# Performance work log

Hardware: AMD Instinct MI355X
Metric: run time of the kernel (lower is better)

Reference implementation:

```python
import jax, jax.numpy as jnp
import numpy as np

HIDDEN = 1024
BATCH = 16
SEQ = 2048
NEG_INF = -1000000000.0


def setup_inputs() -> dict:
    key = jax.random.key(0)
    k1, k2, k3, k4, k5, k6, k7 = jax.random.split(key, 7)
    scale = 1.0 / np.sqrt(HIDDEN)
    return {
        "query": jax.random.normal(k1, (BATCH, HIDDEN), dtype=jnp.float32),
        "keys": jax.random.normal(k2, (BATCH, SEQ, HIDDEN), dtype=jnp.float32),
        "values": jax.random.normal(k3, (BATCH, SEQ, HIDDEN), dtype=jnp.float32),
        "mask": jax.random.randint(k4, (BATCH, SEQ), 0, 2, dtype=jnp.int32),
        # Learned params (nn.Linear(in, out) weight has shape (out, in); we store transposed for x @ W)
        "W1": jax.random.uniform(k5, (HIDDEN, HIDDEN), dtype=jnp.float32, minval=-scale, maxval=scale),
        "W2": jax.random.uniform(k6, (HIDDEN, HIDDEN), dtype=jnp.float32, minval=-scale, maxval=scale),
        "v": jax.random.uniform(k7, (HIDDEN,), dtype=jnp.float32, minval=-scale, maxval=scale),
    }


def reference(query, keys, values, mask, W1, W2, v):
    # scores = v^T tanh(W1 q + W2 k)
    q_proj = query @ W1                       # (b, h)
    k_proj = jnp.einsum('bsh,hd->bsd', keys, W2)  # (b, s, h)
    scores = jnp.einsum('bsh,h->bs', jnp.tanh(q_proj[:, None, :] + k_proj), v)  # (b, s)
    scores = jnp.where(mask == 0, NEG_INF, scores)
    attention_weights = jax.nn.softmax(scores, axis=1)  # (b, s)
    context = jnp.einsum('bs,bsh->bh', attention_weights, values)  # (b, h)
    return context, attention_weights
```

## Files before the change

kernel.cpp:

```cpp
#include <hip/hip_runtime.h>
#include <hip/hip_bf16.h>
#include <cstdint>
#include <cstddef>

#define HIDDEN 1024
#define BATCH 16
#define SEQ 2048
#define M_TOTAL (BATCH*SEQ)
#define NEG_INF -1000000000.0f

typedef unsigned short u16;
typedef __bf16 bf16x8 __attribute__((ext_vector_type(8)));
typedef unsigned short u16x8 __attribute__((ext_vector_type(8)));
typedef unsigned short u16x4 __attribute__((ext_vector_type(4)));
typedef float f32x4 __attribute__((ext_vector_type(4)));

typedef const __attribute__((address_space(1))) void* gas_ptr;
typedef __attribute__((address_space(3))) void* las_ptr;

__device__ __forceinline__ u16 f2bf(float f) {
    unsigned int x = __float_as_uint(f);
    unsigned int r = (x + 0x7fffu + ((x >> 16) & 1u)) >> 16;
    return (u16)r;
}

__device__ __forceinline__ unsigned cvt_pk_bf16(float lo, float hi) {
    unsigned r;
    asm("v_cvt_pk_bf16_f32 %0, %1, %2" : "=v"(r) : "v"(lo), "v"(hi));
    return r;
}

__device__ __forceinline__ float fast_tanh(float x) {
    float e = __expf(2.0f * x);
    return 1.0f - 2.0f / (e + 1.0f);
}

__global__ __launch_bounds__(512) void qproj_kernel(
    const float* __restrict__ q, const float* __restrict__ W1,
    float* __restrict__ qp)
{
    const int b  = blockIdx.y;
    const int tl = threadIdx.x & 63;
    const int kc = threadIdx.x >> 6;
    const int n  = blockIdx.x * 64 + tl;
    __shared__ float red[8][64];

    const float* qrow = q + b * HIDDEN;
    float acc = 0.f;
    #pragma unroll 8
    for (int k = kc * 128; k < kc * 128 + 128; ++k)
        acc += qrow[k] * W1[(size_t)k * HIDDEN + n];
    red[kc][tl] = acc;
    __syncthreads();
    if (kc == 0) {
        float s = 0.f;
        #pragma unroll
        for (int i = 0; i < 8; ++i) s += red[i][tl];
        qp[b * HIDDEN + n] = s;
    }
}

__global__ __launch_bounds__(256) void w2t_kernel(
    const float* __restrict__ W2, u16* __restrict__ W2T)
{
    __shared__ float tile[64][65];
    const int n0 = blockIdx.x * 64, k0 = blockIdx.y * 64;
    const int tid = threadIdx.x;
    const int c = tid & 63, rb = tid >> 6;
    #pragma unroll
    for (int i = 0; i < 16; ++i) {
        int r = rb + i * 4;
        tile[r][c] = W2[(size_t)(k0 + r) * HIDDEN + n0 + c];
    }
    __syncthreads();
    #pragma unroll
    for (int i = 0; i < 16; ++i) {
        int r = rb + i * 4;
        W2T[(size_t)(n0 + r) * HIDDEN + k0 + c] = f2bf(tile[c][r]);
    }
}

#define NT4 16

#define WAITV(N) asm volatile("s_waitcnt vmcnt(" #N ")" ::: "memory")
#define WAITLGKM0 asm volatile("s_waitcnt lgkmcnt(0)" ::: "memory")

#define SBAR() do { __builtin_amdgcn_s_barrier(); \
                    asm volatile("" ::: "memory"); } while (0)

#define A_LOAD(DST, HALF, KT)                                               \
    do {                                                                    \
        _Pragma("unroll")                                                   \
        for (int h_ = 0; h_ < 4; ++h_)                                      \
            DST[h_] = *(const float4*)(keys                                 \
                + (size_t)(m0 + (HALF) * 128 + arow + h_ * 32) * HIDDEN     \
                + (KT) + ac * 4);                                           \
    } while (0)

#define A_WRITE(SRC, LOFF)                                                  \
    do {                                                                    \
        _Pragma("unroll")                                                   \
        for (int h_ = 0; h_ < 4; ++h_) {                                    \
            int row_ = arow + h_ * 32;                                      \
            unsigned lo_ = cvt_pk_bf16(SRC[h_].x, SRC[h_].y);               \
            unsigned hi_ = cvt_pk_bf16(SRC[h_].z, SRC[h_].w);               \
            int byte_ = row_ * 128 + (((ac >> 1) ^ (row_ & 7)) << 4)        \
                        + ((ac & 1) << 3);                                  \
            *(uint2*)((char*)lds + (LOFF) + byte_) = make_uint2(lo_, hi_);  \
        }                                                                   \
    } while (0)

#define STAGE_B(ROW0, KT, LOFF)                                             \
    do {                                                                    \
        _Pragma("unroll")                                                   \
        for (int r_ = 0; r_ < 2; ++r_) {                                    \
            int idx_ = r_ * 512 + tid;                                      \
            int row_ = idx_ >> 3, c_ = idx_ & 7;                            \
            const u16* s_ = W2T + (size_t)(n0 + (ROW0) + row_) * HIDDEN     \
                            + (KT) + ((c_ ^ (row_ & 7)) << 3);              \
            las_ptr d_ = (las_ptr)((char*)lds + (LOFF)                      \
                            + (size_t)(r_ * 512 + (wave << 6)) * 16);       \
            __builtin_amdgcn_global_load_lds((gas_ptr)s_, d_, 16, 0, 0);    \
        }                                                                   \
    } while (0)

#define LDFRAG(LBASE, ROWL, CH) __builtin_bit_cast(bf16x8,                  \
    *(const u16x8*)((LBASE) + (ROWL) * 64 + ((((CH) ^ ((ROWL) & 7))) << 3)))

#define PHASE(MS, NS, LOADA, ...)                                           \
    do {                                                                    \
        if (LOADA) {                                                        \
            _Pragma("unroll")                                               \
            for (int i_ = 0; i_ < 4; ++i_) {                                \
                int rowa_ = (MS) * 128 + wr * 64 + i_ * 16 + c16;           \
                af[i_][0] = LDFRAG(Acur, rowa_, quad);                      \
                af[i_][1] = LDFRAG(Acur, rowa_, 4 + quad);                  \
            }                                                               \
        }                                                                   \
        _Pragma("unroll")                                                   \
        for (int jj_ = 0; jj_ < 2; ++jj_) {                                 \
            int rowb_ = (NS) * 128 + wc * 32 + jj_ * 16 + c16;              \
            bfr[jj_][0] = LDFRAG(Bcur, rowb_, quad);                        \
            bfr[jj_][1] = LDFRAG(Bcur, rowb_, 4 + quad);                    \
        }                                                                   \
        __VA_ARGS__;                                                        \
        SBAR();                                                             \
        __builtin_amdgcn_s_setprio(1);                                      \
        _Pragma("unroll")                                                   \
        for (int i_ = 0; i_ < 4; ++i_)                                      \
            _Pragma("unroll")                                               \
            for (int jj_ = 0; jj_ < 2; ++jj_) {                             \
                acc[MS][i_][NS][jj_] =                                      \
                    __builtin_amdgcn_mfma_f32_16x16x32_bf16(                \
                        af[i_][0], bfr[jj_][0], acc[MS][i_][NS][jj_],0,0,0);\
                acc[MS][i_][NS][jj_] =                                      \
                    __builtin_amdgcn_mfma_f32_16x16x32_bf16(                \
                        af[i_][1], bfr[jj_][1], acc[MS][i_][NS][jj_],0,0,0);\
            }                                                               \
        __builtin_amdgcn_s_setprio(0);                                      \
        SBAR();                                                             \
    } while (0)

__global__ __launch_bounds__(512) void scores_v4_kernel(
    const float* __restrict__ keys,
    const u16*   __restrict__ W2T,
    const float* __restrict__ qp,
    const float* __restrict__ v,
    float*       __restrict__ part)
{
    __shared__ __align__(16) u16 lds[65536];

    const int tid = threadIdx.x;
    const int lid = blockIdx.x + (blockIdx.y << 2);
    const int xcd = lid & 7;
    const int j8  = lid >> 3;
    const int nt  = j8 & 3;
    const int mt  = (xcd << 4) + (j8 >> 2);
    const int m0  = mt << 8;
    const int n0  = nt << 8;

    const int wave = tid >> 6, lane = tid & 63;
    const int wr = wave >> 2;
    const int wc = wave & 3;
    const int quad = lane >> 4, c16 = lane & 15;

    const int arow = tid >> 4;
    const int ac   = tid & 15;

    f32x4 acc[2][4][2][2];
    #pragma unroll
    for (int a = 0; a < 2; ++a)
        #pragma unroll
        for (int i = 0; i < 4; ++i)
            #pragma unroll
            for (int c = 0; c < 2; ++c)
                #pragma unroll
                for (int d = 0; d < 2; ++d)
                    acc[a][i][c][d] = f32x4{0.f, 0.f, 0.f, 0.f};

    bf16x8 af[4][2], bfr[2][2];
    float4 a0[4], a1[4];

    A_LOAD(a0, 0, 0);
    STAGE_B(0, 0, 65536);
    A_LOAD(a1, 1, 0);
    STAGE_B(128, 0, 65536 + 16384);
    WAITV(8);
    A_WRITE(a0, 0);
    WAITV(2);
    A_WRITE(a1, 16384);
    WAITV(0);
    WAITLGKM0;
    SBAR();

    for (int T = 0; T < NT4 - 1; ++T) {
        const int p = T & 1;
        const u16* Acur = (const u16*)((const char*)lds + p * 32768);
        const u16* Bcur = (const u16*)((const char*)lds + 65536 + p * 32768);
        const int aoff = (p ^ 1) * 32768;
        const int boff = 65536 + (p ^ 1) * 32768;
        const int ktn = (T + 1) * 64;

        PHASE(0, 0, true,
              A_LOAD(a0, 0, ktn); STAGE_B(0, ktn, boff); WAITV(6));
        PHASE(0, 1, false,
              WAITV(2); A_WRITE(a0, aoff);
              A_LOAD(a1, 1, ktn); STAGE_B(128, ktn, boff + 16384));
        PHASE(1, 0, true,
              WAITV(2); A_WRITE(a1, aoff + 16384));
        PHASE(1, 1, false,
              WAITLGKM0);
    }
    {
        const u16* Acur = (const u16*)((const char*)lds + 32768);
        const u16* Bcur = (const u16*)((const char*)lds + 65536 + 32768);
        PHASE(0, 0, true,  WAITV(0));
        PHASE(0, 1, false, );
        PHASE(1, 0, true,  );
        PHASE(1, 1, false, );
    }

    const int b = m0 >> 11;
    float qv[2][2], vv[2][2];
    #pragma unroll
    for (int ns = 0; ns < 2; ++ns)
        #pragma unroll
        for (int jj = 0; jj < 2; ++jj) {
            int n = n0 + ns * 128 + wc * 32 + jj * 16 + c16;
            qv[ns][jj] = qp[b * HIDDEN + n];
            vv[ns][jj] = v[n];
        }
    const int slot = (nt << 2) + wc;
    #pragma unroll
    for (int ms = 0; ms < 2; ++ms)
        #pragma unroll
        for (int i = 0; i < 4; ++i)
            #pragma unroll
            for (int r = 0; r < 4; ++r) {
                float s = 0.f;
                #pragma unroll
                for (int ns = 0; ns < 2; ++ns)
                    #pragma unroll
                    for (int jj = 0; jj < 2; ++jj)
                        s += fast_tanh(acc[ms][i][ns][jj][r] + qv[ns][jj])
                             * vv[ns][jj];
                s += __shfl_xor(s, 1);
                s += __shfl_xor(s, 2);
                s += __shfl_xor(s, 4);
                s += __shfl_xor(s, 8);
                if (c16 == 0) {
                    int m = m0 + ms * 128 + wr * 64 + i * 16 + quad * 4 + r;
                    part[(size_t)slot * M_TOTAL + m] = s;
                }
            }
}

#define BM 128
#define BN 128
#define BK 64
#define LDA 72

__global__ __launch_bounds__(256) void scores_v1_kernel(
    const float* __restrict__ keys,
    const u16*   __restrict__ W2T,
    const float* __restrict__ qp,
    const float* __restrict__ v,
    float*       __restrict__ part)
{
    __shared__ __align__(16) u16 Alds[BM][LDA];
    __shared__ __align__(16) u16 Blds[BN][LDA];

    const int tid  = threadIdx.x;
    const int nt   = blockIdx.x;
    const int n0   = nt * BN;
    const int m0   = blockIdx.y * BM;
    const int wave = tid >> 6, lane = tid & 63;
    const int wr = wave >> 1, wc = wave & 1;
    const int quad = lane >> 4, c16 = lane & 15;

    f32x4 acc[4][4];
    #pragma unroll
    for (int i = 0; i < 4; ++i)
        #pragma unroll
        for (int jj = 0; jj < 4; ++jj)
            acc[i][jj] = f32x4{0.f, 0.f, 0.f, 0.f};

    for (int kt = 0; kt < HIDDEN; kt += BK) {
        __syncthreads();
        const float* gA = keys + (size_t)m0 * HIDDEN + kt;
        #pragma unroll
        for (int i = 0; i < 8; ++i) {
            int idx = tid + i * 256;
            int r = idx >> 4, c4 = idx & 15;
            float4 f = *(const float4*)(gA + (size_t)r * HIDDEN + c4 * 4);
            u16x4 pk;
            pk[0] = f2bf(f.x); pk[1] = f2bf(f.y);
            pk[2] = f2bf(f.z); pk[3] = f2bf(f.w);
            *(u16x4*)&Alds[r][c4 * 4] = pk;
        }
        #pragma unroll
        for (int i = 0; i < 4; ++i) {
            int idx = tid + i * 256;
            int r = idx >> 3, c8 = idx & 7;
            uint4 raw = ((const uint4*)(W2T + (size_t)(n0 + r) * HIDDEN + kt))[c8];
            *(uint4*)&Blds[r][c8 * 8] = raw;
        }
        __syncthreads();

        #pragma unroll
        for (int ks = 0; ks < BK; ks += 32) {
            bf16x8 af[4], bfr[4];
            #pragma unroll
            for (int i = 0; i < 4; ++i)
                af[i] = __builtin_bit_cast(bf16x8,
                    *(const u16x8*)&Alds[wr * 64 + i * 16 + c16][ks + quad * 8]);
            #pragma unroll
            for (int jj = 0; jj < 4; ++jj)
                bfr[jj] = __builtin_bit_cast(bf16x8,
                    *(const u16x8*)&Blds[wc * 64 + jj * 16 + c16][ks + quad * 8]);
            #pragma unroll
            for (int i = 0; i < 4; ++i)
                #pragma unroll
                for (int jj = 0; jj < 4; ++jj)
                    acc[i][jj] = __builtin_amdgcn_mfma_f32_16x16x32_bf16(
                        af[i], bfr[jj], acc[i][jj], 0, 0, 0);
        }
    }

    const int b = m0 >> 11;
    float qv[4], vv[4];
    #pragma unroll
    for (int jj = 0; jj < 4; ++jj) {
        int n = n0 + wc * 64 + jj * 16 + c16;
        qv[jj] = qp[b * HIDDEN + n];
        vv[jj] = v[n];
    }
    const int slot = nt * 2 + wc;
    #pragma unroll
    for (int i = 0; i < 4; ++i) {
        #pragma unroll
        for (int r = 0; r < 4; ++r) {
            float s = 0.f;
            #pragma unroll
            for (int jj = 0; jj < 4; ++jj)
                s += fast_tanh(acc[i][jj][r] + qv[jj]) * vv[jj];
            s += __shfl_xor(s, 1);
            s += __shfl_xor(s, 2);
            s += __shfl_xor(s, 4);
            s += __shfl_xor(s, 8);
            if (c16 == 0) {
                int m = m0 + wr * 64 + i * 16 + quad * 4 + r;
                part[(size_t)slot * M_TOTAL + m] = s;
            }
        }
    }
}

__global__ __launch_bounds__(1024) void softmax_kernel(
    const float* __restrict__ part, const int* __restrict__ mask,
    float* __restrict__ attn)
{
    const int b = blockIdx.x, tid = threadIdx.x;
    const int wave = tid >> 6, lane = tid & 63;
    __shared__ float red[16];
    float sc[2];
    float mx = -1e30f;
    #pragma unroll
    for (int j = 0; j < 2; ++j) {
        int s = tid + j * 1024;
        float a = 0.f;
        #pragma unroll
        for (int p = 0; p < 16; ++p)
            a += part[(size_t)p * M_TOTAL + b * SEQ + s];
        if (mask[b * SEQ + s] == 0) a = NEG_INF;
        sc[j] = a;
        mx = fmaxf(mx, a);
    }
    #pragma unroll
    for (int o = 32; o > 0; o >>= 1) mx = fmaxf(mx, __shfl_xor(mx, o));
    if (lane == 0) red[wave] = mx;
    __syncthreads();
    #pragma unroll
    for (int w = 0; w < 16; ++w) mx = fmaxf(mx, red[w]);
    float sum = 0.f;
    #pragma unroll
    for (int j = 0; j < 2; ++j) { sc[j] = __expf(sc[j] - mx); sum += sc[j]; }
    #pragma unroll
    for (int o = 32; o > 0; o >>= 1) sum += __shfl_xor(sum, o);
    __syncthreads();
    if (lane == 0) red[wave] = sum;
    __syncthreads();
    sum = 0.f;
    #pragma unroll
    for (int w = 0; w < 16; ++w) sum += red[w];
    float inv = 1.0f / sum;
    #pragma unroll
    for (int j = 0; j < 2; ++j)
        attn[b * SEQ + tid + j * 1024] = sc[j] * inv;
}

__global__ __launch_bounds__(256) void ctx_part_kernel(
    const float* __restrict__ values, const float* __restrict__ attn,
    float* __restrict__ ctxp)
{
    const int b = blockIdx.x, sch = blockIdx.y, tid = threadIdx.x;
    __shared__ float w[32];
    if (tid < 32) w[tid] = attn[b * SEQ + sch * 32 + tid];
    __syncthreads();
    float4 acc = {0.f, 0.f, 0.f, 0.f};
    const float4* V = (const float4*)(values
        + (size_t)b * SEQ * HIDDEN + (size_t)sch * 32 * HIDDEN);
    #pragma unroll 4
    for (int s = 0; s < 32; ++s) {
        float wv = w[s];
        if (wv != 0.0f) {
            float4 x = V[(size_t)s * (HIDDEN / 4) + tid];
            acc.x += wv * x.x; acc.y += wv * x.y;
            acc.z += wv * x.z; acc.w += wv * x.w;
        }
    }
    ((float4*)(ctxp + (size_t)(b * 64 + sch) * HIDDEN))[tid] = acc;
}

__global__ __launch_bounds__(256) void ctx_reduce_kernel(
    const float* __restrict__ ctxp, float* __restrict__ ctx)
{
    const int b = blockIdx.x, tid = threadIdx.x;
    float4 acc = {0.f, 0.f, 0.f, 0.f};
    const float4* P = (const float4*)(ctxp + (size_t)b * 64 * HIDDEN);
    #pragma unroll 8
    for (int s = 0; s < 64; ++s) {
        float4 x = P[(size_t)s * (HIDDEN / 4) + tid];
        acc.x += x.x; acc.y += x.y; acc.z += x.z; acc.w += x.w;
    }
    ((float4*)(ctx + (size_t)b * HIDDEN))[tid] = acc;
}

extern "C" void kernel_launch(void* const* d_in, const int* in_sizes, int n_in,
                              void* d_out, int out_size, void* d_ws, size_t ws_size,
                              hipStream_t stream)
{
    const float* query  = (const float*)d_in[0];
    const float* keys   = (const float*)d_in[1];
    const float* values = (const float*)d_in[2];
    const int*   mask   = (const int*)d_in[3];
    const float* W1     = (const float*)d_in[4];
    const float* W2     = (const float*)d_in[5];
    const float* v      = (const float*)d_in[6];
    float* out = (float*)d_out;

    char* ws = (char*)d_ws;
    float* qp     = (float*)ws;
    u16*   w2t    = (u16*)(ws + (64 << 10));
    float* part   = (float*)(ws + (64 << 10) + (2 << 20));
    float* ctxp   = (float*)(ws + (64 << 10) + (4 << 20));
    const size_t WS_V4 = (64 << 10) + (8 << 20);

    float* attn_out = out + BATCH * HIDDEN;

    qproj_kernel<<<dim3(16, 16), 512, 0, stream>>>(query, W1, qp);
    w2t_kernel  <<<dim3(16, 16), 256, 0, stream>>>(W2, w2t);

    if (ws_size >= WS_V4) {
        scores_v4_kernel<<<dim3(4, 128), 512, 0, stream>>>(
            keys, w2t, qp, v, part);
        softmax_kernel<<<16, 1024, 0, stream>>>(part, mask, attn_out);
        ctx_part_kernel<<<dim3(16, 64), 256, 0, stream>>>(
            values, attn_out, ctxp);
        ctx_reduce_kernel<<<16, 256, 0, stream>>>(ctxp, out);
    } else {
        scores_v1_kernel<<<dim3(8, 256), 256, 0, stream>>>(
            keys, w2t, qp, v, part);
        softmax_kernel<<<16, 1024, 0, stream>>>(part, mask, attn_out);
        if (ws_size >= (64 << 10) + (8 << 20)) {
            ctx_part_kernel<<<dim3(16, 64), 256, 0, stream>>>(
                values, attn_out, ctxp);
            ctx_reduce_kernel<<<16, 256, 0, stream>>>(ctxp, out);
        } else {
            hipMemsetAsync(d_out, 0, BATCH * HIDDEN * sizeof(float), stream);
            ctx_part_kernel<<<dim3(16, 64), 256, 0, stream>>>(
                values, attn_out, (float*)d_ws);
            ctx_reduce_kernel<<<16, 256, 0, stream>>>((float*)d_ws, out);
        }
    }
}
```

Measured before the change: 401.8 us.

## Prefetch A tiles two iterations ahead with double register buffers in scores kernel

Restructures the scores GEMM main loop so fp32 key (A) tiles are loaded from global memory two K-steps ahead into alternating register buffer sets, while B stays one step ahead in LDS. The loop is unrolled by two and gets a new prologue and epilogue. The aim is to hide global load latency for the large keys stream behind more MFMA work. In exchange it uses more VGPRs (16 float4 held in flight), which may raise register pressure or spill under the 512-thread launch bound.

```diff
diff --git a/kernel.cpp b/kernel.cpp
--- a/kernel.cpp
+++ b/kernel.cpp
@@ -161,7 +161,30 @@
         SBAR();                                                             \
     } while (0)
 
-__global__ __launch_bounds__(512) void scores_v4_kernel(
+#define TILE_BODY(T, LD0, LD1, WR0, WR1)                                    \
+    do {                                                                    \
+        const int p_ = (T) & 1;                                             \
+        const u16* Acur = (const u16*)((const char*)lds + p_ * 32768);      \
+        const u16* Bcur = (const u16*)((const char*)lds + 65536             \
+                                       + p_ * 32768);                       \
+        const int aoff_ = (p_ ^ 1) * 32768;                                 \
+        const int boff_ = 65536 + (p_ ^ 1) * 32768;                         \
+        const int ktL_ = ((T) + 2) * 64;                                    \
+        const int ktB_ = ((T) + 1) * 64;                                    \
+        PHASE(0, 0, true,                                                   \
+              STAGE_B(0, ktB_, boff_);                                      \
+              A_LOAD(LD0, 0, ktL_); A_LOAD(LD1, 1, ktL_);                   \
+              WAITV(10));                                                   \
+        PHASE(0, 1, false,                                                  \
+              A_WRITE(WR0, aoff_);                                          \
+              STAGE_B(128, ktB_, boff_ + 16384));                           \
+        PHASE(1, 0, true,                                                   \
+              A_WRITE(WR1, aoff_ + 16384));                                 \
+        PHASE(1, 1, false,                                                  \
+              WAITLGKM0; WAITV(10));                                        \
+    } while (0)
+
+__global__ __launch_bounds__(512) void scores_v5_kernel(
     const float* __restrict__ keys,
     const u16*   __restrict__ W2T,
     const float* __restrict__ qp,
@@ -199,37 +222,35 @@
                     acc[a][i][c][d] = f32x4{0.f, 0.f, 0.f, 0.f};
 
     bf16x8 af[4][2], bfr[2][2];
-    float4 a0[4], a1[4];
-
-    A_LOAD(a0, 0, 0);
+    float4 aA0[4], aA1[4];
+    float4 aB0[4], aB1[4];
+
+    A_LOAD(aA0, 0, 0);
+    A_LOAD(aA1, 1, 0);
     STAGE_B(0, 0, 65536);
-    A_LOAD(a1, 1, 0);
+    WAITV(2);
+    A_WRITE(aA0, 0);
+    A_WRITE(aA1, 16384);
+    A_LOAD(aB0, 0, 64);
+    A_LOAD(aB1, 1, 64);
     STAGE_B(128, 0, 65536 + 16384);
-    WAITV(8);
-    A_WRITE(a0, 0);
-    WAITV(2);
-    A_WRITE(a1, 16384);
-    WAITV(0);
+    WAITV(10);
     WAITLGKM0;
     SBAR();
 
-    for (int T = 0; T < NT4 - 1; ++T) {
-        const int p = T & 1;
-        const u16* Acur = (const u16*)((const char*)lds + p * 32768);
-        const u16* Bcur = (const u16*)((const char*)lds + 65536 + p * 32768);
-        const int aoff = (p ^ 1) * 32768;
-        const int boff = 65536 + (p ^ 1) * 32768;
-        const int ktn = (T + 1) * 64;
-
-        PHASE(0, 0, true,
-              A_LOAD(a0, 0, ktn); STAGE_B(0, ktn, boff); WAITV(6));
-        PHASE(0, 1, false,
-              WAITV(2); A_WRITE(a0, aoff);
-              A_LOAD(a1, 1, ktn); STAGE_B(128, ktn, boff + 16384));
-        PHASE(1, 0, true,
-              WAITV(2); A_WRITE(a1, aoff + 16384));
-        PHASE(1, 1, false,
-              WAITLGKM0);
+    for (int T = 0; T < 14; T += 2) {
+        TILE_BODY(T,     aA0, aA1, aB0, aB1);
+        TILE_BODY(T + 1, aB0, aB1, aA0, aA1);
+    }
+
+    {
+        const u16* Acur = (const u16*)((const char*)lds);
+        const u16* Bcur = (const u16*)((const char*)lds + 65536);
+        PHASE(0, 0, true,  STAGE_B(0, 960, 65536 + 32768); WAITV(2));
+        PHASE(0, 1, false, A_WRITE(aB0, 32768);
+                           STAGE_B(128, 960, 65536 + 32768 + 16384));
+        PHASE(1, 0, true,  A_WRITE(aB1, 32768 + 16384));
+        PHASE(1, 1, false, WAITLGKM0; WAITV(2));
     }
     {
         const u16* Acur = (const u16*)((const char*)lds + 32768);
@@ -474,15 +495,15 @@
     u16*   w2t    = (u16*)(ws + (64 << 10));
     float* part   = (float*)(ws + (64 << 10) + (2 << 20));
     float* ctxp   = (float*)(ws + (64 << 10) + (4 << 20));
-    const size_t WS_V4 = (64 << 10) + (8 << 20);
+    const size_t WS_V5 = (64 << 10) + (8 << 20);
 
     float* attn_out = out + BATCH * HIDDEN;
 
     qproj_kernel<<<dim3(16, 16), 512, 0, stream>>>(query, W1, qp);
     w2t_kernel  <<<dim3(16, 16), 256, 0, stream>>>(W2, w2t);
 
-    if (ws_size >= WS_V4) {
-        scores_v4_kernel<<<dim3(4, 128), 512, 0, stream>>>(
+    if (ws_size >= WS_V5) {
+        scores_v5_kernel<<<dim3(4, 128), 512, 0, stream>>>(
             keys, w2t, qp, v, part);
         softmax_kernel<<<16, 1024, 0, stream>>>(part, mask, attn_out);
         ctx_part_kernel<<<dim3(16, 64), 256, 0, stream>>>(
```

After: 575.3 us. 1.43x slower.
